# Optimization experiments

Hardware: AMD Instinct MI355X
Metric: run time of the kernel (lower is better)

The kernel has to match this reference:

```python
import jax, jax.numpy as jnp
import numpy as np

B, C, H, W = 4, 128, 128, 128
K = 9          # 3x3 kernel taps
TAU, BETA = 0.5, 10.0


def conv3x3(x, w, b):
    # x: (B,Cin,H,W), w: (Cout,Cin,3,3), stride 1, padding 1
    y = jax.lax.conv_general_dilated(
        x, w, window_strides=(1, 1), padding=((1, 1), (1, 1)),
        dimension_numbers=('NCHW', 'OIHW', 'NCHW'))
    return y + b[None, :, None, None]


def bilinear_sample(x, py, px):
    # x: (B,C,H,W); py,px: (B,K,H,W) fractional coords -> (B,C,K,H,W), zero outside
    Hi, Wi = x.shape[2], x.shape[3]
    y0 = jnp.floor(py); x0 = jnp.floor(px)
    y1 = y0 + 1.0;      x1 = x0 + 1.0
    ly = py - y0; lx = px - x0
    hy = 1.0 - ly; hx = 1.0 - lx
    xf = x.reshape(x.shape[0], x.shape[1], -1)  # (B,C,HW)

    def corner(yc, xc, wgt):
        valid = (yc >= 0) & (yc <= Hi - 1) & (xc >= 0) & (xc <= Wi - 1)
        yi = jnp.clip(yc, 0, Hi - 1).astype(jnp.int32)
        xi = jnp.clip(xc, 0, Wi - 1).astype(jnp.int32)
        idx = (yi * Wi + xi).reshape(yc.shape[0], -1)  # (B, K*H*W)
        g = jax.vmap(lambda f, i: f[:, i])(xf, idx)    # (B,C,K*H*W)
        g = g.reshape(x.shape[0], x.shape[1], *yc.shape[1:])  # (B,C,K,H,W)
        return g * (wgt * valid.astype(wgt.dtype))[:, None]

    return (corner(y0, x0, hy * hx) + corner(y0, x1, hy * lx)
            + corner(y1, x0, ly * hx) + corner(y1, x1, ly * lx))


def modulated_dcn(x, offset, mask, w, b):
    # offset: (B,2K,H,W) layout (dy,dx) per tap; mask: (B,K,H,W)
    Bn, Cn, Hn, Wn = x.shape
    off = offset.reshape(Bn, K, 2, Hn, Wn)
    dy, dx = off[:, :, 0], off[:, :, 1]
    ky, kx = jnp.meshgrid(jnp.arange(3), jnp.arange(3), indexing='ij')
    base_y = (ky.reshape(-1) - 1).astype(x.dtype)  # dilation=1, padding=1, stride=1
    base_x = (kx.reshape(-1) - 1).astype(x.dtype)
    hh = jnp.arange(Hn, dtype=x.dtype)
    ww = jnp.arange(Wn, dtype=x.dtype)
    py = hh[None, None, :, None] + base_y[None, :, None, None] + dy  # (B,K,H,W)
    px = ww[None, None, None, :] + base_x[None, :, None, None] + dx
    samp = bilinear_sample(x, py, px) * mask[:, None]  # (B,C,K,H,W)
    out = jnp.einsum('bckhw,ock->bohw', samp, w.reshape(w.shape[0], w.shape[1], K))
    return out + b[None, :, None, None]


def setup_inputs() -> dict:
    key = jax.random.key(0)
    ks = jax.random.split(key, 8)
    x = jax.random.normal(ks[0], (B, C, H, W), dtype=jnp.float32)
    U = jax.random.uniform(ks[1], (B, 1, H, W), dtype=jnp.float32)
    # conv_offset_mask: (3*K, C+1, 3, 3); small scale -> offsets of O(1) pixel
    w_om = jax.random.normal(ks[2], (3 * K, C + 1, 3, 3), dtype=jnp.float32) * 0.01
    b_om = jnp.zeros((3 * K,), dtype=jnp.float32)
    kaiming = float(np.sqrt(2.0 / (C * 9)))
    w_dcn = jax.random.normal(ks[3], (C, C, 3, 3), dtype=jnp.float32) * kaiming
    b_dcn = jnp.zeros((C,), dtype=jnp.float32)
    w1 = jax.random.normal(ks[4], (C, C, 3, 3), dtype=jnp.float32) * kaiming
    b1 = jnp.zeros((C,), dtype=jnp.float32)
    w2 = jax.random.normal(ks[5], (C, C, 3, 3), dtype=jnp.float32) * float(np.sqrt(1.0 / (C * 9)))
    b2 = jnp.zeros((C,), dtype=jnp.float32)
    return {"x": x, "U": U, "w_om": w_om, "b_om": b_om, "w_dcn": w_dcn,
            "b_dcn": b_dcn, "w1": w1, "b1": b1, "w2": w2, "b2": b2}


def reference(x, U, w_om, b_om, w_dcn, b_dcn, w1, b1, w2, b2):
    U = jnp.clip(U, 0.0, 1.0)
    guide = jnp.concatenate([x, U], axis=1)                # (B,C+1,H,W)
    om = conv3x3(guide, w_om, b_om)                        # (B,3K,H,W)
    offset = om[:, :2 * K]
    mask = 2.0 * jax.nn.sigmoid(om[:, 2 * K:])
    z = modulated_dcn(x, offset, mask, w_dcn, b_dcn)
    r = jax.nn.relu(conv3x3(z, w1, b1))
    r = conv3x3(r, w2, b2)
    gate = jax.nn.sigmoid(BETA * (U - TAU))
    return jax.nn.relu(x + r * gate)
```

## Files before the change

kernel.cpp:

```cpp
#include <hip/hip_runtime.h>
#include <math.h>

typedef unsigned int uint;
typedef unsigned short ushort;
typedef __attribute__((ext_vector_type(8))) __bf16 bf16x8;
typedef __attribute__((ext_vector_type(4))) float f32x4;

#define HW 16384

__device__ __forceinline__ ushort f2bf(float f) {
    uint u = __float_as_uint(f);
    u += 0x7fffu + ((u >> 16) & 1u);
    return (ushort)(u >> 16);
}
__device__ __forceinline__ void bhmap(int& b, int& h) {
    int lin = blockIdx.y * (int)gridDim.x + blockIdx.x;
    int n = (lin & 7) * 64 + (lin >> 3);
    h = n & 127;
    b = n >> 7;
}
__device__ __forceinline__ int swz(int row, int chunk) {
    return row * 128 + ((chunk ^ (row & 15)) << 3);
}
__device__ __forceinline__ uint blend2(uint a, uint b, uint c, uint d,
                                       float w00, float w01, float w10, float w11) {
    float lo = w00 * __uint_as_float(a << 16) + w01 * __uint_as_float(b << 16)
             + w10 * __uint_as_float(c << 16) + w11 * __uint_as_float(d << 16);
    float hi = w00 * __uint_as_float(a & 0xffff0000u) + w01 * __uint_as_float(b & 0xffff0000u)
             + w10 * __uint_as_float(c & 0xffff0000u) + w11 * __uint_as_float(d & 0xffff0000u);
    uint ul = __float_as_uint(lo); ul += 0x7fffu + ((ul >> 16) & 1u);
    uint uh = __float_as_uint(hi); uh += 0x7fffu + ((uh >> 16) & 1u);
    return (ul >> 16) | ((uh >> 16) << 16);
}

__global__ __launch_bounds__(256) void prep_w(
    const float* __restrict__ wd, const float* __restrict__ w1,
    const float* __restrict__ w2, const float* __restrict__ wom,
    ushort* __restrict__ wdt, ushort* __restrict__ w1t,
    ushort* __restrict__ w2t, ushort* __restrict__ womt,
    float* __restrict__ womu)
{
    int i = blockIdx.x * 256 + threadIdx.x;
    if (i < 147456) {
        int k = i >> 14, oc = (i >> 7) & 127, ci = i & 127;
        int s = (oc * 128 + ci) * 9 + k;
        wdt[i] = f2bf(wd[s]);
        w1t[i] = f2bf(w1[s]);
        w2t[i] = f2bf(w2[s]);
    }
    if (i < 36864) {
        int k = i >> 12, oc = (i >> 7) & 31, ci = i & 127;
        womt[i] = (oc < 27) ? f2bf(wom[(oc * 129 + ci) * 9 + k]) : (ushort)0;
    }
    if (i < 288) {
        int k = i >> 5, oc = i & 31;
        womu[i] = (oc < 27) ? wom[(oc * 129 + 128) * 9 + k] : 0.f;
    }
}

__global__ __launch_bounds__(256) void prep_xt(
    const float* __restrict__ x, ushort* __restrict__ xt)
{
    int b, h; bhmap(b, h);
    const int tid = threadIdx.x;
    __shared__ __align__(16) ushort T[128 * 136];
    const int w0 = tid & 127, cg = tid >> 7;
#pragma unroll 4
    for (int it = 0; it < 64; it++) {
        int c = it * 2 + cg;
        float f = x[((size_t)(b * 128 + c)) * HW + h * 128 + w0];
        T[w0 * 136 + c] = f2bf(f);
    }
    __syncthreads();
    const int w1 = tid >> 1, half = tid & 1;
    uint4* dst = (uint4*)(xt + (((size_t)b * HW) + h * 128 + w1) * 128 + half * 64);
    const uint4* src = (const uint4*)&T[w1 * 136 + half * 64];
#pragma unroll
    for (int c8 = 0; c8 < 8; c8++) dst[c8] = src[c8];
}

__global__ __launch_bounds__(512, 4) void k_om(
    const ushort* __restrict__ xt, const float* __restrict__ U,
    const ushort* __restrict__ womt, const float* __restrict__ womu,
    const float* __restrict__ bom, float* __restrict__ omt)
{
    int b, h; bhmap(b, h);
    const int tid = threadIdx.x;
    const int wid = tid >> 6, lane = tid & 63, lq = lane & 15, quad = lane >> 4;
    const int pixbase = wid * 16;

    __shared__ __align__(16) ushort As[128 * 128];
    __shared__ __align__(16) ushort Bs[32 * 128];
    __shared__ float U3[3 * 130];
    __shared__ float wu[288];

    f32x4 acc[2];
#pragma unroll
    for (int j = 0; j < 2; j++)
#pragma unroll
        for (int r = 0; r < 4; r++) acc[j][r] = 0.f;

    for (int s = tid; s < 390; s += 512) {
        int r = s / 130, c = s % 130, gy = h - 1 + r, gx = c - 1;
        float v = 0.f;
        if ((unsigned)gy < 128u && (unsigned)gx < 128u) {
            v = U[(size_t)b * HW + gy * 128 + gx];
            v = fminf(fmaxf(v, 0.f), 1.f);
        }
        U3[s] = v;
    }
    if (tid < 288) wu[tid] = womu[tid];

    const int arow = tid >> 2, aq = tid & 3;
    const int brow = tid >> 4, bchunk = tid & 15;
    for (int t9 = 0; t9 < 9; t9++) {
        int dy = t9 / 3 - 1, dx = t9 % 3 - 1;
        int gy = h + dy, gx = arow + dx;
        if ((unsigned)gy < 128u && (unsigned)gx < 128u) {
            const uint4* src = (const uint4*)(xt + (((size_t)b * HW) + gy * 128 + gx) * 128 + aq * 32);
#pragma unroll
            for (int c = 0; c < 4; c++) *(uint4*)&As[swz(arow, aq * 4 + c)] = src[c];
        } else {
            uint4 zz = {0, 0, 0, 0};
#pragma unroll
            for (int c = 0; c < 4; c++) *(uint4*)&As[swz(arow, aq * 4 + c)] = zz;
        }
        *(uint4*)&Bs[swz(brow, bchunk)] = *(const uint4*)(womt + t9 * 4096 + brow * 128 + bchunk * 8);
        __syncthreads();
#pragma unroll
        for (int kk = 0; kk < 4; kk++) {
            int chunk = kk * 4 + quad;
            bf16x8 av = *(const bf16x8*)&As[swz(pixbase + lq, chunk)];
            bf16x8 bv[2];
#pragma unroll
            for (int j = 0; j < 2; j++) bv[j] = *(const bf16x8*)&Bs[swz(j * 16 + lq, chunk)];
#pragma unroll
            for (int j = 0; j < 2; j++)
                acc[j] = __builtin_amdgcn_mfma_f32_16x16x32_bf16(av, bv[j], acc[j], 0, 0, 0);
        }
        __syncthreads();
    }

#pragma unroll
    for (int j = 0; j < 2; j++) {
        int oc = j * 16 + lq;
        if (oc < 27) {
            float bias = bom[oc];
#pragma unroll
            for (int r = 0; r < 4; r++) {
                int pix = pixbase + quad * 4 + r;
                float v = acc[j][r] + bias;
#pragma unroll
                for (int t = 0; t < 9; t++)
                    v += U3[(t / 3) * 130 + pix + (t % 3)] * wu[t * 32 + oc];
                if (oc >= 18) v = 2.f / (1.f + __expf(-v));
                omt[((size_t)b * HW + h * 128 + pix) * 32 + oc] = v;
            }
        }
    }
}

__global__ __launch_bounds__(512, 4) void k_dcn(
    const ushort* __restrict__ xt, const float* __restrict__ omt,
    const ushort* __restrict__ wdt, const float* __restrict__ bdcn,
    ushort* __restrict__ zt)
{
    int b, h; bhmap(b, h);
    const int tid = threadIdx.x;
    const int wid = tid >> 6, lane = tid & 63, lq = lane & 15, quad = lane >> 4;
    const int pixbase = (wid & 1) * 64, ocbase = (wid >> 1) * 32;

    __shared__ __align__(16) ushort As[128 * 128];
    __shared__ __align__(16) ushort Bs[128 * 128];
    __shared__ __align__(16) int tbl[2][128][8];

    const int sc = lane & 15;
    const int sp = lane >> 4;

    f32x4 acc[4][2];
#pragma unroll
    for (int i = 0; i < 4; i++)
#pragma unroll
        for (int j = 0; j < 2; j++)
#pragma unroll
            for (int r = 0; r < 4; r++) acc[i][j][r] = 0.f;

    const float* omrow = omt + ((size_t)b * HW + h * 128) * 32;
    const ushort* xtb = xt + (size_t)b * HW * 128;

    auto build = [&](int k, int buf) {
        if (tid < 128) {
            int p = tid;
            float dyv = omrow[p * 32 + 2 * k];
            float dxv = omrow[p * 32 + 2 * k + 1];
            float m   = omrow[p * 32 + 18 + k];
            float fy = (float)(h + k / 3 - 1) + dyv;
            float fx = (float)(p + k % 3 - 1) + dxv;
            float y0f = floorf(fy), x0f = floorf(fx);
            float ly = fy - y0f, lx = fx - x0f;
            float hy = 1.f - ly, hx = 1.f - lx;
            bool vy0 = (y0f >= 0.f) && (y0f <= 127.f);
            bool vy1 = (y0f >= -1.f) && (y0f <= 126.f);
            bool vx0 = (x0f >= 0.f) && (x0f <= 127.f);
            bool vx1 = (x0f >= -1.f) && (x0f <= 126.f);
            float w00 = (vy0 && vx0) ? hy * hx * m : 0.f;
            float w01 = (vy0 && vx1) ? hy * lx * m : 0.f;
            float w10 = (vy1 && vx0) ? ly * hx * m : 0.f;
            float w11 = (vy1 && vx1) ? ly * lx * m : 0.f;
            int iy0 = min(max((int)y0f, 0), 127);
            int iy1 = min(max((int)y0f + 1, 0), 127);
            int ix0 = min(max((int)x0f, 0), 127);
            int ix1 = min(max((int)x0f + 1, 0), 127);
            int* tp = &tbl[buf][p][0];
            tp[0] = (iy0 * 128 + ix0) * 128;
            tp[1] = (iy0 * 128 + ix1) * 128;
            tp[2] = (iy1 * 128 + ix0) * 128;
            tp[3] = (iy1 * 128 + ix1) * 128;
            ((float*)tp)[4] = w00; ((float*)tp)[5] = w01;
            ((float*)tp)[6] = w10; ((float*)tp)[7] = w11;
        }
    };

    build(0, 0);
    __syncthreads();

    const int brow = tid >> 2, bq = tid & 3;
    for (int k = 0; k < 9; k++) {
        const int buf = k & 1;
        {
            const uint4* src = (const uint4*)(wdt + (size_t)k * 16384 + brow * 128 + bq * 32);
#pragma unroll
            for (int c = 0; c < 4; c++) *(uint4*)&Bs[swz(brow, bq * 4 + c)] = src[c];
        }
        const ushort* basep = xtb + sc * 8;
#pragma unroll 2
        for (int r = 0; r < 4; r++) {
            int p = r * 32 + wid * 4 + sp;
            int4 off = *(const int4*)&tbl[buf][p][0];
            f32x4 wv = *(const f32x4*)((const float*)&tbl[buf][p][0] + 4);
            uint4 q00 = *(const uint4*)(basep + off.x);
            uint4 q01 = *(const uint4*)(basep + off.y);
            uint4 q10 = *(const uint4*)(basep + off.z);
            uint4 q11 = *(const uint4*)(basep + off.w);
            uint4 st;
            st.x = blend2(q00.x, q01.x, q10.x, q11.x, wv[0], wv[1], wv[2], wv[3]);
            st.y = blend2(q00.y, q01.y, q10.y, q11.y, wv[0], wv[1], wv[2], wv[3]);
            st.z = blend2(q00.z, q01.z, q10.z, q11.z, wv[0], wv[1], wv[2], wv[3]);
            st.w = blend2(q00.w, q01.w, q10.w, q11.w, wv[0], wv[1], wv[2], wv[3]);
            *(uint4*)&As[swz(p, sc)] = st;
        }
        __syncthreads();
        if (k < 8) build(k + 1, buf ^ 1);
#pragma unroll
        for (int kk = 0; kk < 4; kk++) {
            int chunk = kk * 4 + quad;
            bf16x8 av[4], bv[2];
#pragma unroll
            for (int i = 0; i < 4; i++) av[i] = *(const bf16x8*)&As[swz(pixbase + i * 16 + lq, chunk)];
#pragma unroll
            for (int j = 0; j < 2; j++) bv[j] = *(const bf16x8*)&Bs[swz(ocbase + j * 16 + lq, chunk)];
#pragma unroll
            for (int i = 0; i < 4; i++)
#pragma unroll
                for (int j = 0; j < 2; j++)
                    acc[i][j] = __builtin_amdgcn_mfma_f32_16x16x32_bf16(av[i], bv[j], acc[i][j], 0, 0, 0);
        }
        __syncthreads();
    }

    size_t prow = ((size_t)b * HW + h * 128) * 128;
#pragma unroll
    for (int j = 0; j < 2; j++) {
        int oc = ocbase + j * 16 + lq;
        float bias = bdcn[oc];
#pragma unroll
        for (int i = 0; i < 4; i++)
#pragma unroll
            for (int r = 0; r < 4; r++) {
                int pix = pixbase + i * 16 + quad * 4 + r;
                zt[prow + (size_t)pix * 128 + oc] = f2bf(acc[i][j][r] + bias);
            }
    }
}

__global__ __launch_bounds__(512, 4) void k_conv1(
    const ushort* __restrict__ zt, const ushort* __restrict__ w1t,
    const float* __restrict__ b1, ushort* __restrict__ r1t)
{
    int b, h; bhmap(b, h);
    const int tid = threadIdx.x;
    const int wid = tid >> 6, lane = tid & 63, lq = lane & 15, quad = lane >> 4;
    const int pixbase = (wid & 1) * 64, ocbase = (wid >> 1) * 32;

    __shared__ __align__(16) ushort As[128 * 128];
    __shared__ __align__(16) ushort Bs[128 * 128];

    f32x4 acc[4][2];
#pragma unroll
    for (int i = 0; i < 4; i++)
#pragma unroll
        for (int j = 0; j < 2; j++)
#pragma unroll
            for (int r = 0; r < 4; r++) acc[i][j][r] = 0.f;

    const int row = tid >> 2, q = tid & 3;
    for (int t9 = 0; t9 < 9; t9++) {
        int dy = t9 / 3 - 1, dx = t9 % 3 - 1;
        int gy = h + dy, gx = row + dx;
        if ((unsigned)gy < 128u && (unsigned)gx < 128u) {
            const uint4* src = (const uint4*)(zt + (((size_t)b * HW) + gy * 128 + gx) * 128 + q * 32);
#pragma unroll
            for (int c = 0; c < 4; c++) *(uint4*)&As[swz(row, q * 4 + c)] = src[c];
        } else {
            uint4 zz = {0, 0, 0, 0};
#pragma unroll
            for (int c = 0; c < 4; c++) *(uint4*)&As[swz(row, q * 4 + c)] = zz;
        }
        {
            const uint4* src = (const uint4*)(w1t + (size_t)t9 * 16384 + row * 128 + q * 32);
#pragma unroll
            for (int c = 0; c < 4; c++) *(uint4*)&Bs[swz(row, q * 4 + c)] = src[c];
        }
        __syncthreads();
#pragma unroll
        for (int kk = 0; kk < 4; kk++) {
            int chunk = kk * 4 + quad;
            bf16x8 av[4], bv[2];
#pragma unroll
            for (int i = 0; i < 4; i++) av[i] = *(const bf16x8*)&As[swz(pixbase + i * 16 + lq, chunk)];
#pragma unroll
            for (int j = 0; j < 2; j++) bv[j] = *(const bf16x8*)&Bs[swz(ocbase + j * 16 + lq, chunk)];
#pragma unroll
            for (int i = 0; i < 4; i++)
#pragma unroll
                for (int j = 0; j < 2; j++)
                    acc[i][j] = __builtin_amdgcn_mfma_f32_16x16x32_bf16(av[i], bv[j], acc[i][j], 0, 0, 0);
        }
        __syncthreads();
    }

    size_t prow = ((size_t)b * HW + h * 128) * 128;
#pragma unroll
    for (int j = 0; j < 2; j++) {
        int oc = ocbase + j * 16 + lq;
        float bias = b1[oc];
#pragma unroll
        for (int i = 0; i < 4; i++)
#pragma unroll
            for (int r = 0; r < 4; r++) {
                int pix = pixbase + i * 16 + quad * 4 + r;
                r1t[prow + (size_t)pix * 128 + oc] = f2bf(fmaxf(acc[i][j][r] + bias, 0.f));
            }
    }
}

__global__ __launch_bounds__(512, 4) void k_conv2(
    const ushort* __restrict__ r1t, const ushort* __restrict__ w2t,
    const float* __restrict__ b2, const float* __restrict__ x,
    const float* __restrict__ U, float* __restrict__ out)
{
    int b, h; bhmap(b, h);
    const int tid = threadIdx.x;
    const int wid = tid >> 6, lane = tid & 63, lq = lane & 15, quad = lane >> 4;
    const int mbase = (wid & 1) * 64;
    const int nbase = (wid >> 1) * 32;

    __shared__ __align__(16) ushort As[128 * 128];
    __shared__ __align__(16) ushort Bs[128 * 128];

    f32x4 acc[4][2];
#pragma unroll
    for (int i = 0; i < 4; i++)
#pragma unroll
        for (int j = 0; j < 2; j++)
#pragma unroll
            for (int r = 0; r < 4; r++) acc[i][j][r] = 0.f;

    const int row = tid >> 2, q = tid & 3;
    for (int t9 = 0; t9 < 9; t9++) {
        int dy = t9 / 3 - 1, dx = t9 % 3 - 1;
        {
            const uint4* src = (const uint4*)(w2t + (size_t)t9 * 16384 + row * 128 + q * 32);
#pragma unroll
            for (int c = 0; c < 4; c++) *(uint4*)&As[swz(row, q * 4 + c)] = src[c];
        }
        int gy = h + dy, gx = row + dx;
        if ((unsigned)gy < 128u && (unsigned)gx < 128u) {
            const uint4* src = (const uint4*)(r1t + (((size_t)b * HW) + gy * 128 + gx) * 128 + q * 32);
#pragma unroll
            for (int c = 0; c < 4; c++) *(uint4*)&Bs[swz(row, q * 4 + c)] = src[c];
        } else {
            uint4 zz = {0, 0, 0, 0};
#pragma unroll
            for (int c = 0; c < 4; c++) *(uint4*)&Bs[swz(row, q * 4 + c)] = zz;
        }
        __syncthreads();
#pragma unroll
        for (int kk = 0; kk < 4; kk++) {
            int chunk = kk * 4 + quad;
            bf16x8 av[4], bv[2];
#pragma unroll
            for (int i = 0; i < 4; i++) av[i] = *(const bf16x8*)&As[swz(mbase + i * 16 + lq, chunk)];
#pragma unroll
            for (int j = 0; j < 2; j++) bv[j] = *(const bf16x8*)&Bs[swz(nbase + j * 16 + lq, chunk)];
#pragma unroll
            for (int i = 0; i < 4; i++)
#pragma unroll
                for (int j = 0; j < 2; j++)
                    acc[i][j] = __builtin_amdgcn_mfma_f32_16x16x32_bf16(av[i], bv[j], acc[i][j], 0, 0, 0);
        }
        __syncthreads();
    }

#pragma unroll
    for (int j = 0; j < 2; j++) {
        int pix = nbase + j * 16 + lq;
        float u = U[(size_t)b * HW + h * 128 + pix];
        u = fminf(fmaxf(u, 0.f), 1.f);
        float g = 1.f / (1.f + __expf(-10.f * (u - 0.5f)));
#pragma unroll
        for (int i = 0; i < 4; i++) {
            f32x4 b4 = *(const f32x4*)&b2[mbase + i * 16 + quad * 4];
#pragma unroll
            for (int r = 0; r < 4; r++) {
                int oc = mbase + i * 16 + quad * 4 + r;
                size_t idx = ((size_t)(b * 128 + oc)) * HW + h * 128 + pix;
                float v = acc[i][j][r] + b4[r];
                out[idx] = fmaxf(x[idx] + v * g, 0.f);
            }
        }
    }
}

extern "C" void kernel_launch(void* const* d_in, const int* in_sizes, int n_in,
                              void* d_out, int out_size, void* d_ws, size_t ws_size,
                              hipStream_t stream)
{
    const float* x     = (const float*)d_in[0];
    const float* U     = (const float*)d_in[1];
    const float* w_om  = (const float*)d_in[2];
    const float* b_om  = (const float*)d_in[3];
    const float* w_dcn = (const float*)d_in[4];
    const float* b_dcn = (const float*)d_in[5];
    const float* w1    = (const float*)d_in[6];
    const float* b1    = (const float*)d_in[7];
    const float* w2    = (const float*)d_in[8];
    const float* b2    = (const float*)d_in[9];
    float* out = (float*)d_out;

    char* p = (char*)d_ws;
    ushort* xt   = (ushort*)p; p += (size_t)4 * HW * 128 * 2;
    ushort* zt   = (ushort*)p; p += (size_t)4 * HW * 128 * 2;
    ushort* r1t  = (ushort*)p; p += (size_t)4 * HW * 128 * 2;
    float*  omt  = (float*)p;  p += (size_t)4 * HW * 32 * 4;
    ushort* wdt  = (ushort*)p; p += 147456 * 2;
    ushort* w1t  = (ushort*)p; p += 147456 * 2;
    ushort* w2t  = (ushort*)p; p += 147456 * 2;
    ushort* womt = (ushort*)p; p += 36864 * 2;
    float*  womu = (float*)p;  p += 288 * 4;

    prep_w<<<576, 256, 0, stream>>>(w_dcn, w1, w2, w_om, wdt, w1t, w2t, womt, womu);
    prep_xt<<<dim3(128, 4), 256, 0, stream>>>(x, xt);
    k_om<<<dim3(128, 4), 512, 0, stream>>>(xt, U, womt, womu, b_om, omt);
    k_dcn<<<dim3(128, 4), 512, 0, stream>>>(xt, omt, wdt, b_dcn, zt);
    k_conv1<<<dim3(128, 4), 512, 0, stream>>>(zt, w1t, b1, r1t);
    k_conv2<<<dim3(128, 4), 512, 0, stream>>>(r1t, w2t, b2, x, U, out);
}
```

Measured before the change: 233.9 us.

## Load conv weight fragments directly from global into registers, drop LDS staging

In the DCN, conv1 and conv2 kernels the weight tile is no longer staged through a 32KB shared-memory buffer. Each wave loads its own MFMA weight fragments straight from global memory, which hit L2 because every block reads the same weights. This halves LDS use per block, which can raise occupancy, and removes the LDS write and read traffic for weights. The cost is more global load instructions, and in conv2 those loads sit inside the MFMA loop, so their latency may be exposed.

```diff
diff --git a/kernel.cpp b/kernel.cpp
--- a/kernel.cpp
+++ b/kernel.cpp
@@ -171,7 +171,6 @@
     const int pixbase = (wid & 1) * 64, ocbase = (wid >> 1) * 32;
 
     __shared__ __align__(16) ushort As[128 * 128];
-    __shared__ __align__(16) ushort Bs[128 * 128];
     __shared__ __align__(16) int tbl[2][128][8];
 
     const int sc = lane & 15;
@@ -201,7 +200,7 @@
             float hy = 1.f - ly, hx = 1.f - lx;
             bool vy0 = (y0f >= 0.f) && (y0f <= 127.f);
             bool vy1 = (y0f >= -1.f) && (y0f <= 126.f);
-            bool vx0 = (x0f >= 0.f) && (x0f <= 127.f);
+        bool vx0 = (x0f >= 0.f) && (x0f <= 127.f);
             bool vx1 = (x0f >= -1.f) && (x0f <= 126.f);
             float w00 = (vy0 && vx0) ? hy * hx * m : 0.f;
             float w01 = (vy0 && vx1) ? hy * lx * m : 0.f;
@@ -224,14 +223,16 @@
     build(0, 0);
     __syncthreads();
 
-    const int brow = tid >> 2, bq = tid & 3;
     for (int k = 0; k < 9; k++) {
         const int buf = k & 1;
-        {
-            const uint4* src = (const uint4*)(wdt + (size_t)k * 16384 + brow * 128 + bq * 32);
-#pragma unroll
-            for (int c = 0; c < 4; c++) *(uint4*)&Bs[swz(brow, bq * 4 + c)] = src[c];
-        }
+        const ushort* wp = wdt + (size_t)k * 16384 + (ocbase + lq) * 128 + quad * 8;
+        bf16x8 bv[2][4];
+#pragma unroll
+        for (int j = 0; j < 2; j++)
+#pragma unroll
+            for (int kk = 0; kk < 4; kk++)
+                bv[j][kk] = *(const bf16x8*)(wp + j * 2048 + kk * 32);
+
         const ushort* basep = xtb + sc * 8;
 #pragma unroll 2
         for (int r = 0; r < 4; r++) {
@@ -254,16 +255,14 @@
 #pragma unroll
         for (int kk = 0; kk < 4; kk++) {
             int chunk = kk * 4 + quad;
-            bf16x8 av[4], bv[2];
+            bf16x8 av[4];
 #pragma unroll
             for (int i = 0; i < 4; i++) av[i] = *(const bf16x8*)&As[swz(pixbase + i * 16 + lq, chunk)];
 #pragma unroll
-            for (int j = 0; j < 2; j++) bv[j] = *(const bf16x8*)&Bs[swz(ocbase + j * 16 + lq, chunk)];
-#pragma unroll
             for (int i = 0; i < 4; i++)
 #pragma unroll
                 for (int j = 0; j < 2; j++)
-                    acc[i][j] = __builtin_amdgcn_mfma_f32_16x16x32_bf16(av[i], bv[j], acc[i][j], 0, 0, 0);
+                    acc[i][j] = __builtin_amdgcn_mfma_f32_16x16x32_bf16(av[i], bv[j][kk], acc[i][j], 0, 0, 0);
         }
         __syncthreads();
     }
@@ -293,7 +292,6 @@
     const int pixbase = (wid & 1) * 64, ocbase = (wid >> 1) * 32;
 
     __shared__ __align__(16) ushort As[128 * 128];
-    __shared__ __align__(16) ushort Bs[128 * 128];
 
     f32x4 acc[4][2];
 #pragma unroll
@@ -306,6 +304,14 @@
     const int row = tid >> 2, q = tid & 3;
     for (int t9 = 0; t9 < 9; t9++) {
         int dy = t9 / 3 - 1, dx = t9 % 3 - 1;
+        const ushort* wp = w1t + (size_t)t9 * 16384 + (ocbase + lq) * 128 + quad * 8;
+        bf16x8 bv[2][4];
+#pragma unroll
+        for (int j = 0; j < 2; j++)
+#pragma unroll
+            for (int kk = 0; kk < 4; kk++)
+                bv[j][kk] = *(const bf16x8*)(wp + j * 2048 + kk * 32);
+
         int gy = h + dy, gx = row + dx;
         if ((unsigned)gy < 128u && (unsigned)gx < 128u) {
             const uint4* src = (const uint4*)(zt + (((size_t)b * HW) + gy * 128 + gx) * 128 + q * 32);
@@ -316,25 +322,18 @@
 #pragma unroll
             for (int c = 0; c < 4; c++) *(uint4*)&As[swz(row, q * 4 + c)] = zz;
         }
-        {
-            const uint4* src = (const uint4*)(w1t + (size_t)t9 * 16384 + row * 128 + q * 32);
-#pragma unroll
-            for (int c = 0; c < 4; c++) *(uint4*)&Bs[swz(row, q * 4 + c)] = src[c];
-        }
         __syncthreads();
 #pragma unroll
         for (int kk = 0; kk < 4; kk++) {
             int chunk = kk * 4 + quad;
-            bf16x8 av[4], bv[2];
+            bf16x8 av[4];
 #pragma unroll
             for (int i = 0; i < 4; i++) av[i] = *(const bf16x8*)&As[swz(pixbase + i * 16 + lq, chunk)];
 #pragma unroll
-            for (int j = 0; j < 2; j++) bv[j] = *(const bf16x8*)&Bs[swz(ocbase + j * 16 + lq, chunk)];
-#pragma unroll
             for (int i = 0; i < 4; i++)
 #pragma unroll
                 for (int j = 0; j < 2; j++)
-                    acc[i][j] = __builtin_amdgcn_mfma_f32_16x16x32_bf16(av[i], bv[j], acc[i][j], 0, 0, 0);
+                    acc[i][j] = __builtin_amdgcn_mfma_f32_16x16x32_bf16(av[i], bv[j][kk], acc[i][j], 0, 0, 0);
         }
         __syncthreads();
     }
@@ -365,7 +364,6 @@
     const int mbase = (wid & 1) * 64;
     const int nbase = (wid >> 1) * 32;
 
-    __shared__ __align__(16) ushort As[128 * 128];
     __shared__ __align__(16) ushort Bs[128 * 128];
 
     f32x4 acc[4][2];
@@ -379,11 +377,8 @@
     const int row = tid >> 2, q = tid & 3;
     for (int t9 = 0; t9 < 9; t9++) {
         int dy = t9 / 3 - 1, dx = t9 % 3 - 1;
-        {
-            const uint4* src = (const uint4*)(w2t + (size_t)t9 * 16384 + row * 128 + q * 32);
-#pragma unroll
-            for (int c = 0; c < 4; c++) *(uint4*)&As[swz(row, q * 4 + c)] = src[c];
-        }
+        const ushort* wp = w2t + (size_t)t9 * 16384 + (mbase + lq) * 128 + quad * 8;
+
         int gy = h + dy, gx = row + dx;
         if ((unsigned)gy < 128u && (unsigned)gx < 128u) {
             const uint4* src = (const uint4*)(r1t + (((size_t)b * HW) + gy * 128 + gx) * 128 + q * 32);
@@ -398,16 +393,17 @@
 #pragma unroll
         for (int kk = 0; kk < 4; kk++) {
             int chunk = kk * 4 + quad;
-            bf16x8 av[4], bv[2];
-#pragma unroll
-            for (int i = 0; i < 4; i++) av[i] = *(const bf16x8*)&As[swz(mbase + i * 16 + lq, chunk)];
-#pragma unroll
-            for (int j = 0; j < 2; j++) bv[j] = *(const bf16x8*)&Bs[swz(nbase + j * 16 + lq, chunk)];
+            bf16x8 av[4], bvv[2];
 #pragma unroll
             for (int i = 0; i < 4; i++)
+                av[i] = *(const bf16x8*)(wp + i * 2048 + kk * 32);
+#pragma unroll
+            for (int j = 0; j < 2; j++) bvv[j] = *(const bf16x8*)&Bs[swz(nbase + j * 16 + lq, chunk)];
+#pragma unroll
+            for (int i = 0; i < 4; i++)
 #pragma unroll
                 for (int j = 0; j < 2; j++)
-                    acc[i][j] = __builtin_amdgcn_mfma_f32_16x16x32_bf16(av[i], bv[j], acc[i][j], 0, 0, 0);
+                    acc[i][j] = __builtin_amdgcn_mfma_f32_16x16x32_bf16(av[i], bvv[j], acc[i][j], 0, 0, 0);
         }
         __syncthreads();
     }
```

Measured after the change: 326.6 us. 1.4x slower.

## Split DCN and conv kernels into half-row tiles to double block count

Applied to the files above, without the earlier changes.

The DCN, conv1 and conv2 kernels now each process 64 pixels of an image row per block instead of 128, and launch twice as many blocks (1024 vs 512). A new block-to-(batch,row,half) mapping is added, and the LDS tiles, accumulators and load assignments shrink to match. This is meant to fill the 256 CUs of the MI355X better, since 512 blocks leave many CUs with uneven work, and to raise the occupancy hint to 6 blocks per CU. The cost is that every block reloads the full 128x128 weight tile per tap, so weight traffic doubles and each loaded tile feeds fewer MFMAs.

```diff
diff --git a/kernel.cpp b/kernel.cpp
--- a/kernel.cpp
+++ b/kernel.cpp
@@ -18,6 +18,13 @@
     int n = (lin & 7) * 64 + (lin >> 3);
     h = n & 127;
     b = n >> 7;
+}
+__device__ __forceinline__ void bhmap2(int& b, int& h, int& po) {
+    int lin = blockIdx.y * (int)gridDim.x + blockIdx.x;
+    int n = (lin & 7) * 128 + (lin >> 3);
+    po = (n & 1) * 64;
+    h = (n >> 1) & 127;
+    b = n >> 8;
 }
 __device__ __forceinline__ int swz(int row, int chunk) {
     return row * 128 + ((chunk ^ (row & 15)) << 3);
@@ -160,26 +167,26 @@
     }
 }
 
-__global__ __launch_bounds__(512, 4) void k_dcn(
+__global__ __launch_bounds__(512, 6) void k_dcn(
     const ushort* __restrict__ xt, const float* __restrict__ omt,
     const ushort* __restrict__ wdt, const float* __restrict__ bdcn,
     ushort* __restrict__ zt)
 {
-    int b, h; bhmap(b, h);
+    int b, h, po; bhmap2(b, h, po);
     const int tid = threadIdx.x;
     const int wid = tid >> 6, lane = tid & 63, lq = lane & 15, quad = lane >> 4;
-    const int pixbase = (wid & 1) * 64, ocbase = (wid >> 1) * 32;
-
-    __shared__ __align__(16) ushort As[128 * 128];
+    const int pixlocal = (wid & 1) * 32, ocbase = (wid >> 1) * 32;
+
+    __shared__ __align__(16) ushort As[64 * 128];
     __shared__ __align__(16) ushort Bs[128 * 128];
-    __shared__ __align__(16) int tbl[2][128][8];
+    __shared__ __align__(16) int tbl[2][64][8];
 
     const int sc = lane & 15;
     const int sp = lane >> 4;
 
-    f32x4 acc[4][2];
-#pragma unroll
-    for (int i = 0; i < 4; i++)
+    f32x4 acc[2][2];
+#pragma unroll
+    for (int i = 0; i < 2; i++)
 #pragma unroll
         for (int j = 0; j < 2; j++)
 #pragma unroll
@@ -189,13 +196,14 @@
     const ushort* xtb = xt + (size_t)b * HW * 128;
 
     auto build = [&](int k, int buf) {
-        if (tid < 128) {
+        if (tid < 64) {
             int p = tid;
-            float dyv = omrow[p * 32 + 2 * k];
-            float dxv = omrow[p * 32 + 2 * k + 1];
-            float m   = omrow[p * 32 + 18 + k];
+            int gp = po + p;
+            float dyv = omrow[gp * 32 + 2 * k];
+            float dxv = omrow[gp * 32 + 2 * k + 1];
+            float m   = omrow[gp * 32 + 18 + k];
             float fy = (float)(h + k / 3 - 1) + dyv;
-            float fx = (float)(p + k % 3 - 1) + dxv;
+            float fx = (float)(gp + k % 3 - 1) + dxv;
             float y0f = floorf(fy), x0f = floorf(fx);
             float ly = fy - y0f, lx = fx - x0f;
             float hy = 1.f - ly, hx = 1.f - lx;
@@ -233,8 +241,8 @@
             for (int c = 0; c < 4; c++) *(uint4*)&Bs[swz(brow, bq * 4 + c)] = src[c];
         }
         const ushort* basep = xtb + sc * 8;
-#pragma unroll 2
-        for (int r = 0; r < 4; r++) {
+#pragma unroll
+        for (int r = 0; r < 2; r++) {
             int p = r * 32 + wid * 4 + sp;
             int4 off = *(const int4*)&tbl[buf][p][0];
             f32x4 wv = *(const f32x4*)((const float*)&tbl[buf][p][0] + 4);
@@ -254,13 +262,13 @@
 #pragma unroll
         for (int kk = 0; kk < 4; kk++) {
             int chunk = kk * 4 + quad;
-            bf16x8 av[4], bv[2];
-#pragma unroll
-            for (int i = 0; i < 4; i++) av[i] = *(const bf16x8*)&As[swz(pixbase + i * 16 + lq, chunk)];
+            bf16x8 av[2], bv[2];
+#pragma unroll
+            for (int i = 0; i < 2; i++) av[i] = *(const bf16x8*)&As[swz(pixlocal + i * 16 + lq, chunk)];
 #pragma unroll
             for (int j = 0; j < 2; j++) bv[j] = *(const bf16x8*)&Bs[swz(ocbase + j * 16 + lq, chunk)];
 #pragma unroll
-            for (int i = 0; i < 4; i++)
+            for (int i = 0; i < 2; i++)
 #pragma unroll
                 for (int j = 0; j < 2; j++)
                     acc[i][j] = __builtin_amdgcn_mfma_f32_16x16x32_bf16(av[i], bv[j], acc[i][j], 0, 0, 0);
@@ -274,64 +282,65 @@
         int oc = ocbase + j * 16 + lq;
         float bias = bdcn[oc];
 #pragma unroll
-        for (int i = 0; i < 4; i++)
+        for (int i = 0; i < 2; i++)
 #pragma unroll
             for (int r = 0; r < 4; r++) {
-                int pix = pixbase + i * 16 + quad * 4 + r;
+                int pix = po + pixlocal + i * 16 + quad * 4 + r;
                 zt[prow + (size_t)pix * 128 + oc] = f2bf(acc[i][j][r] + bias);
             }
     }
 }
 
-__global__ __launch_bounds__(512, 4) void k_conv1(
+__global__ __launch_bounds__(512, 6) void k_conv1(
     const ushort* __restrict__ zt, const ushort* __restrict__ w1t,
     const float* __restrict__ b1, ushort* __restrict__ r1t)
 {
-    int b, h; bhmap(b, h);
+    int b, h, po; bhmap2(b, h, po);
     const int tid = threadIdx.x;
     const int wid = tid >> 6, lane = tid & 63, lq = lane & 15, quad = lane >> 4;
-    const int pixbase = (wid & 1) * 64, ocbase = (wid >> 1) * 32;
-
-    __shared__ __align__(16) ushort As[128 * 128];
+    const int pixlocal = (wid & 1) * 32, ocbase = (wid >> 1) * 32;
+
+    __shared__ __align__(16) ushort As[64 * 128];
     __shared__ __align__(16) ushort Bs[128 * 128];
 
-    f32x4 acc[4][2];
-#pragma unroll
-    for (int i = 0; i < 4; i++)
+    f32x4 acc[2][2];
+#pragma unroll
+    for (int i = 0; i < 2; i++)
 #pragma unroll
         for (int j = 0; j < 2; j++)
 #pragma unroll
             for (int r = 0; r < 4; r++) acc[i][j][r] = 0.f;
 
-    const int row = tid >> 2, q = tid & 3;
+    const int arow = tid >> 3, aq = tid & 7;
+    const int brow = tid >> 2, bq = tid & 3;
     for (int t9 = 0; t9 < 9; t9++) {
         int dy = t9 / 3 - 1, dx = t9 % 3 - 1;
-        int gy = h + dy, gx = row + dx;
+        int gy = h + dy, gx = po + arow + dx;
         if ((unsigned)gy < 128u && (unsigned)gx < 128u) {
-            const uint4* src = (const uint4*)(zt + (((size_t)b * HW) + gy * 128 + gx) * 128 + q * 32);
-#pragma unroll
-            for (int c = 0; c < 4; c++) *(uint4*)&As[swz(row, q * 4 + c)] = src[c];
+            const uint4* src = (const uint4*)(zt + (((size_t)b * HW) + gy * 128 + gx) * 128 + aq * 16);
+#pragma unroll
+            for (int c = 0; c < 2; c++) *(uint4*)&As[swz(arow, aq * 2 + c)] = src[c];
         } else {
             uint4 zz = {0, 0, 0, 0};
 #pragma unroll
-            for (int c = 0; c < 4; c++) *(uint4*)&As[swz(row, q * 4 + c)] = zz;
+            for (int c = 0; c < 2; c++) *(uint4*)&As[swz(arow, aq * 2 + c)] = zz;
         }
         {
-            const uint4* src = (const uint4*)(w1t + (size_t)t9 * 16384 + row * 128 + q * 32);
-#pragma unroll
-            for (int c = 0; c < 4; c++) *(uint4*)&Bs[swz(row, q * 4 + c)] = src[c];
+            const uint4* src = (const uint4*)(w1t + (size_t)t9 * 16384 + brow * 128 + bq * 32);
+#pragma unroll
+            for (int c = 0; c < 4; c++) *(uint4*)&Bs[swz(brow, bq * 4 + c)] = src[c];
         }
         __syncthreads();
 #pragma unroll
         for (int kk = 0; kk < 4; kk++) {
             int chunk = kk * 4 + quad;
-            bf16x8 av[4], bv[2];
-#pragma unroll
-            for (int i = 0; i < 4; i++) av[i] = *(const bf16x8*)&As[swz(pixbase + i * 16 + lq, chunk)];
+            bf16x8 av[2], bv[2];
+#pragma unroll
+            for (int i = 0; i < 2; i++) av[i] = *(const bf16x8*)&As[swz(pixlocal + i * 16 + lq, chunk)];
 #pragma unroll
             for (int j = 0; j < 2; j++) bv[j] = *(const bf16x8*)&Bs[swz(ocbase + j * 16 + lq, chunk)];
 #pragma unroll
-            for (int i = 0; i < 4; i++)
+            for (int i = 0; i < 2; i++)
 #pragma unroll
                 for (int j = 0; j < 2; j++)
                     acc[i][j] = __builtin_amdgcn_mfma_f32_16x16x32_bf16(av[i], bv[j], acc[i][j], 0, 0, 0);
@@ -345,66 +354,67 @@
         int oc = ocbase + j * 16 + lq;
         float bias = b1[oc];
 #pragma unroll
-        for (int i = 0; i < 4; i++)
+        for (int i = 0; i < 2; i++)
 #pragma unroll
             for (int r = 0; r < 4; r++) {
-                int pix = pixbase + i * 16 + quad * 4 + r;
+                int pix = po + pixlocal + i * 16 + quad * 4 + r;
                 r1t[prow + (size_t)pix * 128 + oc] = f2bf(fmaxf(acc[i][j][r] + bias, 0.f));
             }
     }
 }
 
-__global__ __launch_bounds__(512, 4) void k_conv2(
+__global__ __launch_bounds__(512, 6) void k_conv2(
     const ushort* __restrict__ r1t, const ushort* __restrict__ w2t,
     const float* __restrict__ b2, const float* __restrict__ x,
     const float* __restrict__ U, float* __restrict__ out)
 {
-    int b, h; bhmap(b, h);
+    int b, h, po; bhmap2(b, h, po);
     const int tid = threadIdx.x;
     const int wid = tid >> 6, lane = tid & 63, lq = lane & 15, quad = lane >> 4;
-    const int mbase = (wid & 1) * 64;
-    const int nbase = (wid >> 1) * 32;
+    const int mbase = (wid >> 1) * 32;
+    const int nbase = (wid & 1) * 32;
 
     __shared__ __align__(16) ushort As[128 * 128];
-    __shared__ __align__(16) ushort Bs[128 * 128];
-
-    f32x4 acc[4][2];
-#pragma unroll
-    for (int i = 0; i < 4; i++)
+    __shared__ __align__(16) ushort Bs[64 * 128];
+
+    f32x4 acc[2][2];
+#pragma unroll
+    for (int i = 0; i < 2; i++)
 #pragma unroll
         for (int j = 0; j < 2; j++)
 #pragma unroll
             for (int r = 0; r < 4; r++) acc[i][j][r] = 0.f;
 
-    const int row = tid >> 2, q = tid & 3;
+    const int arow = tid >> 2, aq = tid & 3;
+    const int brow = tid >> 3, bq = tid & 7;
     for (int t9 = 0; t9 < 9; t9++) {
         int dy = t9 / 3 - 1, dx = t9 % 3 - 1;
         {
-            const uint4* src = (const uint4*)(w2t + (size_t)t9 * 16384 + row * 128 + q * 32);
-#pragma unroll
-            for (int c = 0; c < 4; c++) *(uint4*)&As[swz(row, q * 4 + c)] = src[c];
-        }
-        int gy = h + dy, gx = row + dx;
+            const uint4* src = (const uint4*)(w2t + (size_t)t9 * 16384 + arow * 128 + aq * 32);
+#pragma unroll
+            for (int c = 0; c < 4; c++) *(uint4*)&As[swz(arow, aq * 4 + c)] = src[c];
+        }
+        int gy = h + dy, gx = po + brow + dx;
         if ((unsigned)gy < 128u && (unsigned)gx < 128u) {
-            const uint4* src = (const uint4*)(r1t + (((size_t)b * HW) + gy * 128 + gx) * 128 + q * 32);
-#pragma unroll
-            for (int c = 0; c < 4; c++) *(uint4*)&Bs[swz(row, q * 4 + c)] = src[c];
+            const uint4* src = (const uint4*)(r1t + (((size_t)b * HW) + gy * 128 + gx) * 128 + bq * 16);
+#pragma unroll
+            for (int c = 0; c < 2; c++) *(uint4*)&Bs[swz(brow, bq * 2 + c)] = src[c];
         } else {
             uint4 zz = {0, 0, 0, 0};
 #pragma unroll
-            for (int c = 0; c < 4; c++) *(uint4*)&Bs[swz(row, q * 4 + c)] = zz;
+            for (int c = 0; c < 2; c++) *(uint4*)&Bs[swz(brow, bq * 2 + c)] = zz;
         }
         __syncthreads();
 #pragma unroll
         for (int kk = 0; kk < 4; kk++) {
             int chunk = kk * 4 + quad;
-            bf16x8 av[4], bv[2];
-#pragma unroll
-            for (int i = 0; i < 4; i++) av[i] = *(const bf16x8*)&As[swz(mbase + i * 16 + lq, chunk)];
+            bf16x8 av[2], bv[2];
+#pragma unroll
+            for (int i = 0; i < 2; i++) av[i] = *(const bf16x8*)&As[swz(mbase + i * 16 + lq, chunk)];
 #pragma unroll
             for (int j = 0; j < 2; j++) bv[j] = *(const bf16x8*)&Bs[swz(nbase + j * 16 + lq, chunk)];
 #pragma unroll
-            for (int i = 0; i < 4; i++)
+            for (int i = 0; i < 2; i++)
 #pragma unroll
                 for (int j = 0; j < 2; j++)
                     acc[i][j] = __builtin_amdgcn_mfma_f32_16x16x32_bf16(av[i], bv[j], acc[i][j], 0, 0, 0);
@@ -414,12 +424,12 @@
 
 #pragma unroll
     for (int j = 0; j < 2; j++) {
-        int pix = nbase + j * 16 + lq;
+        int pix = po + nbase + j * 16 + lq;
         float u = U[(size_t)b * HW + h * 128 + pix];
         u = fminf(fmaxf(u, 0.f), 1.f);
         float g = 1.f / (1.f + __expf(-10.f * (u - 0.5f)));
 #pragma unroll
-        for (int i = 0; i < 4; i++) {
+        for (int i = 0; i < 2; i++) {
             f32x4 b4 = *(const f32x4*)&b2[mbase + i * 16 + quad * 4];
 #pragma unroll
             for (int r = 0; r < 4; r++) {
@@ -462,7 +472,7 @@
     prep_w<<<576, 256, 0, stream>>>(w_dcn, w1, w2, w_om, wdt, w1t, w2t, womt, womu);
     prep_xt<<<dim3(128, 4), 256, 0, stream>>>(x, xt);
     k_om<<<dim3(128, 4), 512, 0, stream>>>(xt, U, womt, womu, b_om, omt);
-    k_dcn<<<dim3(128, 4), 512, 0, stream>>>(xt, omt, wdt, b_dcn, zt);
-    k_conv1<<<dim3(128, 4), 512, 0, stream>>>(zt, w1t, b1, r1t);
-    k_conv2<<<dim3(128, 4), 512, 0, stream>>>(r1t, w2t, b2, x, U, out);
-}
+    k_dcn<<<dim3(256, 4), 512, 0, stream>>>(xt, omt, wdt, b_dcn, zt);
+    k_conv1<<<dim3(256, 4), 512, 0, stream>>>(zt, w1t, b1, r1t);
+    k_conv2<<<dim3(256, 4), 512, 0, stream>>>(r1t, w2t, b2, x, U, out);
+}
```

Result: slower. 265.5 us (+13.5%).
